# Kernel optimization log

Hardware: AMD Instinct MI355X
Metric: run time of the kernel (lower is better)

## Reference

```python
import jax, jax.numpy as jnp
import numpy as np

NUM_CLASSES = 10
TEMPERATURE = 10.0
EPS = 1e-8


def _centers_counts(feat, label):
    # segment mean per class; counts used for validity masks
    counts = jax.ops.segment_sum(jnp.ones((feat.shape[0],), feat.dtype), label, NUM_CLASSES)
    sums = jax.ops.segment_sum(feat, label, NUM_CLASSES)
    centers = sums / jnp.maximum(counts, 1.0)[:, None]
    return centers, counts


def setup_inputs() -> dict:
    key = jax.random.key(0)
    k1, k2, k3, k4 = jax.random.split(key, 4)
    N, D = 262144, 64
    return {
        "feat1": jax.random.normal(k1, (N, D), dtype=jnp.float32),
        "label1": jax.random.randint(k2, (N,), 0, NUM_CLASSES, dtype=jnp.int32),
        "feat2": jax.random.normal(k3, (N, D), dtype=jnp.float32),
        "label2": jax.random.randint(k4, (N,), 0, NUM_CLASSES, dtype=jnp.int32),
    }


def reference(feat1, label1, feat2, label2):
    centers1, counts1 = _centers_counts(feat1, label1)   # [C, D], [C]
    centers2, counts2 = _centers_counts(feat2, label2)

    # per-sample euclidean distance to own class center
    d1 = jnp.sqrt(jnp.sum((feat1 - centers1[label1]) ** 2, axis=1))  # [N1]
    d2 = jnp.sqrt(jnp.sum((feat2 - centers2[label2]) ** 2, axis=1))  # [N2]

    # per-class mean distances (segment mean)
    m1 = jax.ops.segment_sum(d1, label1, NUM_CLASSES) / jnp.maximum(counts1, 1.0)
    m2 = jax.ops.segment_sum(d2, label2, NUM_CLASSES) / jnp.maximum(counts2, 1.0)

    # intra: only classes (present in label1, as torch.unique(label1)) with >1 members in both
    valid_intra = (counts1 > 1.0) & (counts2 > 1.0)
    intra_dist = jnp.sum(jnp.where(valid_intra, m1 + m2, 0.0))

    # inter: centers for classes present in both domains; mean over all pairwise distances
    valid_c = (counts1 > 0.0) & (counts2 > 0.0)  # [C]
    diff = centers1[:, None, :] - centers2[None, :, :]  # [C, C, D]
    pd = jnp.sqrt(jnp.sum(diff ** 2, axis=-1))           # [C, C]
    w = (valid_c[:, None] & valid_c[None, :]).astype(pd.dtype)
    n_valid = jnp.sum(valid_c.astype(pd.dtype))
    inter_dist = jnp.where(
        n_valid > 1.0,
        jnp.sum(pd * w) / jnp.maximum(n_valid * n_valid, 1.0),
        0.0,
    )

    normalized = intra_dist / (inter_dist + EPS)
    loss = jnp.where(
        inter_dist > 0.0,
        jnp.log1p(jnp.exp(normalized / TEMPERATURE)),
        intra_dist,
    )
    return loss
```

## Files before the change

### kernel.cpp

```cpp
#include <hip/hip_runtime.h>
#include <math.h>

#define NUM_CLASSES 10
#define D 64

#define PART_FLOATS 1320
#define OFF_SUMS1 0
#define OFF_SUMS2 640
#define OFF_CNT1  1280
#define OFF_CNT2  1290
#define OFF_DSUM1 1300
#define OFF_DSUM2 1310
#define CTR_FLOATS 1300
#define CTR_OFF_C1   0
#define CTR_OFF_C2   640
#define CTR_OFF_CNT1 1280
#define CTR_OFF_CNT2 1290

__global__ void k_zero(float* __restrict__ ws, int npart) {
    int total = npart * PART_FLOATS;
    for (int i = threadIdx.x + blockIdx.x * blockDim.x; i < total; i += blockDim.x * gridDim.x)
        ws[i] = 0.0f;
}

__global__ void k_pass1(const float* __restrict__ f1, const int* __restrict__ l1,
                        const float* __restrict__ f2, const int* __restrict__ l2,
                        int N, float* __restrict__ ws, int npart) {
    const float* f; const int* l; int base_s, base_c;
    if (blockIdx.y == 0) { f = f1; l = l1; base_s = OFF_SUMS1; base_c = OFF_CNT1; }
    else                 { f = f2; l = l2; base_s = OFF_SUMS2; base_c = OFF_CNT2; }
    float* wpart = ws + (size_t)(blockIdx.x & (npart - 1)) * PART_FLOATS;

    __shared__ float accum[4][NUM_CLASSES * D];
    __shared__ float cshare[4][16];
    const int wv   = threadIdx.x >> 6;
    const int lane = threadIdx.x & 63;
    float* acc = accum[wv];

    for (int i = threadIdx.x; i < 4 * NUM_CLASSES * D; i += blockDim.x)
        (&accum[0][0])[i] = 0.0f;
    __syncthreads();

    const int wid   = blockIdx.x * 4 + wv;
    const int nwave = gridDim.x * 4;
    float vcnt = 0.0f;

    for (int r0 = wid * 64; r0 < N; r0 += nwave * 64) {
        int labv = l[min(r0 + lane, N - 1)];
        int nrows = min(64, N - r0);
        for (int rr = 0; rr < 64; rr += 16) {
            float v[16];
#pragma unroll
            for (int k = 0; k < 16; ++k) {
                int ra = min(r0 + rr + k, N - 1);
                v[k] = f[(size_t)ra * D + lane];
            }
#pragma unroll
            for (int k = 0; k < 16; ++k) {
                int r = rr + k;
                if (r < nrows) {
                    int lab = __shfl(labv, r);
                    acc[lab * D + lane] += v[k];
                    vcnt += (lane == lab) ? 1.0f : 0.0f;
                }
            }
        }
    }

    if (lane < NUM_CLASSES) cshare[wv][lane] = vcnt;
    __syncthreads();

    for (int i = threadIdx.x; i < NUM_CLASSES * D; i += blockDim.x) {
        float s = accum[0][i] + accum[1][i] + accum[2][i] + accum[3][i];
        atomicAdd(&wpart[base_s + i], s);
    }
    if (threadIdx.x < NUM_CLASSES) {
        float s = cshare[0][threadIdx.x] + cshare[1][threadIdx.x]
                + cshare[2][threadIdx.x] + cshare[3][threadIdx.x];
        atomicAdd(&wpart[base_c + threadIdx.x], s);
    }
}

__global__ void k_centers(const float* __restrict__ ws, int npart, float* __restrict__ gctr) {
    int dom = blockIdx.x;
    int base_s = dom ? OFF_SUMS2 : OFF_SUMS1;
    int base_c = dom ? OFF_CNT2  : OFF_CNT1;
    int out_c  = dom ? CTR_OFF_C2 : CTR_OFF_C1;
    int out_n  = dom ? CTR_OFF_CNT2 : CTR_OFF_CNT1;
    __shared__ float cnts[NUM_CLASSES];
    if (threadIdx.x < NUM_CLASSES) {
        float a0 = 0.f, a1 = 0.f, a2 = 0.f, a3 = 0.f;
        int p = 0;
        for (; p + 4 <= npart; p += 4) {
            a0 += ws[(p + 0) * PART_FLOATS + base_c + threadIdx.x];
            a1 += ws[(p + 1) * PART_FLOATS + base_c + threadIdx.x];
            a2 += ws[(p + 2) * PART_FLOATS + base_c + threadIdx.x];
            a3 += ws[(p + 3) * PART_FLOATS + base_c + threadIdx.x];
        }
        float cn = (a0 + a1) + (a2 + a3);
        for (; p < npart; ++p) cn += ws[p * PART_FLOATS + base_c + threadIdx.x];
        cnts[threadIdx.x] = cn;
        gctr[out_n + threadIdx.x] = cn;
    }
    __syncthreads();
    int i = threadIdx.x;
    if (i < NUM_CLASSES * D) {
        float a0 = 0.f, a1 = 0.f, a2 = 0.f, a3 = 0.f, a4 = 0.f, a5 = 0.f, a6 = 0.f, a7 = 0.f;
        int p = 0;
        for (; p + 8 <= npart; p += 8) {
            a0 += ws[(p + 0) * PART_FLOATS + base_s + i];
            a1 += ws[(p + 1) * PART_FLOATS + base_s + i];
            a2 += ws[(p + 2) * PART_FLOATS + base_s + i];
            a3 += ws[(p + 3) * PART_FLOATS + base_s + i];
            a4 += ws[(p + 4) * PART_FLOATS + base_s + i];
            a5 += ws[(p + 5) * PART_FLOATS + base_s + i];
            a6 += ws[(p + 6) * PART_FLOATS + base_s + i];
            a7 += ws[(p + 7) * PART_FLOATS + base_s + i];
        }
        float s = ((a0 + a1) + (a2 + a3)) + ((a4 + a5) + (a6 + a7));
        for (; p < npart; ++p) s += ws[p * PART_FLOATS + base_s + i];
        gctr[out_c + i] = s / fmaxf(cnts[i >> 6], 1.0f);
    }
}

__global__ void k_pass2(const float* __restrict__ f1, const int* __restrict__ l1,
                        const float* __restrict__ f2, const int* __restrict__ l2,
                        int N, float* __restrict__ ws, int npart,
                        const float* __restrict__ gctr) {
    const float* f; const int* l; int base_d, ctr_off;
    if (blockIdx.y == 0) { f = f1; l = l1; base_d = OFF_DSUM1; ctr_off = CTR_OFF_C1; }
    else                 { f = f2; l = l2; base_d = OFF_DSUM2; ctr_off = CTR_OFF_C2; }
    float* wpart = ws + (size_t)(blockIdx.x & (npart - 1)) * PART_FLOATS;

    __shared__ float4 ctr[NUM_CLASSES * 17];
    __shared__ float  ld[NUM_CLASSES];
    float* ctrf = reinterpret_cast<float*>(ctr);
    for (int i = threadIdx.x; i < NUM_CLASSES * D; i += blockDim.x)
        ctrf[(i >> 6) * 68 + (i & 63)] = gctr[ctr_off + i];
    if (threadIdx.x < NUM_CLASSES) ld[threadIdx.x] = 0.f;
    __syncthreads();

    const int j = threadIdx.x & 3;
    int g       = blockIdx.x * (blockDim.x >> 2) + (threadIdx.x >> 2);
    const int G = gridDim.x * (blockDim.x >> 2);
    const float4* f4 = reinterpret_cast<const float4*>(f);

    for (int row = g; row < N; row += G) {
        int lab = l[row];
        size_t rb = (size_t)row * 16;
        float4 v0 = f4[rb + 0 + j];
        float4 v1 = f4[rb + 4 + j];
        float4 v2 = f4[rb + 8 + j];
        float4 v3 = f4[rb + 12 + j];
        const float4* cc = &ctr[lab * 17];
        float4 c0 = cc[0 + j], c1 = cc[4 + j], c2 = cc[8 + j], c3 = cc[12 + j];
        float s = 0.f, x;
        x = v0.x - c0.x; s = fmaf(x, x, s); x = v0.y - c0.y; s = fmaf(x, x, s);
        x = v0.z - c0.z; s = fmaf(x, x, s); x = v0.w - c0.w; s = fmaf(x, x, s);
        x = v1.x - c1.x; s = fmaf(x, x, s); x = v1.y - c1.y; s = fmaf(x, x, s);
        x = v1.z - c1.z; s = fmaf(x, x, s); x = v1.w - c1.w; s = fmaf(x, x, s);
        x = v2.x - c2.x; s = fmaf(x, x, s); x = v2.y - c2.y; s = fmaf(x, x, s);
        x = v2.z - c2.z; s = fmaf(x, x, s); x = v2.w - c2.w; s = fmaf(x, x, s);
        x = v3.x - c3.x; s = fmaf(x, x, s); x = v3.y - c3.y; s = fmaf(x, x, s);
        x = v3.z - c3.z; s = fmaf(x, x, s); x = v3.w - c3.w; s = fmaf(x, x, s);
        s += __shfl_xor(s, 1);
        s += __shfl_xor(s, 2);
        if (j == 0) atomicAdd(&ld[lab], sqrtf(s));
    }
    __syncthreads();
    if (threadIdx.x < NUM_CLASSES)
        atomicAdd(&wpart[base_d + threadIdx.x], ld[threadIdx.x]);
}

__global__ void k_final(const float* __restrict__ ws, int npart,
                        const float* __restrict__ gctr, float* __restrict__ out) {
    __shared__ float cnt1[NUM_CLASSES], cnt2[NUM_CLASSES], ds1[NUM_CLASSES], ds2[NUM_CLASSES];
    __shared__ float pd[NUM_CLASSES * NUM_CLASSES];

    if (threadIdx.x < 2 * NUM_CLASSES) {
        int which = threadIdx.x / NUM_CLASSES, c = threadIdx.x % NUM_CLASSES;
        int off = (which == 0 ? OFF_DSUM1 : OFF_DSUM2) + c;
        float s = 0.f;
        for (int p = 0; p < npart; ++p) s += ws[p * PART_FLOATS + off];
        (which == 0 ? ds1 : ds2)[c] = s;
        (which == 0 ? cnt1 : cnt2)[c] = gctr[(which == 0 ? CTR_OFF_CNT1 : CTR_OFF_CNT2) + c];
    }
    __syncthreads();

    if (threadIdx.x < NUM_CLASSES * NUM_CLASSES) {
        int i = threadIdx.x / NUM_CLASSES;
        int j = threadIdx.x % NUM_CLASSES;
        float s = 0.f;
        for (int d = 0; d < D; ++d) {
            float df = gctr[CTR_OFF_C1 + i * D + d] - gctr[CTR_OFF_C2 + j * D + d];
            s += df * df;
        }
        pd[threadIdx.x] = sqrtf(s);
    }
    __syncthreads();

    if (threadIdx.x == 0) {
        float intra = 0.f;
        for (int c = 0; c < NUM_CLASSES; ++c) {
            if (cnt1[c] > 1.0f && cnt2[c] > 1.0f) {
                float m1 = ds1[c] / fmaxf(cnt1[c], 1.0f);
                float m2 = ds2[c] / fmaxf(cnt2[c], 1.0f);
                intra += m1 + m2;
            }
        }
        float n_valid = 0.f;
        for (int i = 0; i < NUM_CLASSES; ++i)
            if (cnt1[i] > 0.0f && cnt2[i] > 0.0f) n_valid += 1.0f;
        float inter_sum = 0.f;
        for (int i = 0; i < NUM_CLASSES; ++i) {
            bool vi = cnt1[i] > 0.0f && cnt2[i] > 0.0f;
            for (int j = 0; j < NUM_CLASSES; ++j) {
                bool vj = cnt1[j] > 0.0f && cnt2[j] > 0.0f;
                if (vi && vj) inter_sum += pd[i * NUM_CLASSES + j];
            }
        }
        float inter = (n_valid > 1.0f) ? inter_sum / fmaxf(n_valid * n_valid, 1.0f) : 0.0f;
        float normalized = intra / (inter + 1e-8f);
        float x = normalized / 10.0f;
        float softplus = (x > 0.0f) ? (x + log1pf(expf(-x))) : log1pf(expf(x));
        float loss = (inter > 0.0f) ? softplus : intra;
        out[0] = loss;
    }
}

extern "C" void kernel_launch(void* const* d_in, const int* in_sizes, int n_in,
                              void* d_out, int out_size, void* d_ws, size_t ws_size,
                              hipStream_t stream) {
    const float* f1 = (const float*)d_in[0];
    const int*   l1 = (const int*)d_in[1];
    const float* f2 = (const float*)d_in[2];
    const int*   l2 = (const int*)d_in[3];
    float* ws  = (float*)d_ws;
    float* out = (float*)d_out;
    const int N = in_sizes[1];

    int npart = 1;
    while (npart < 64 &&
           (size_t)(npart * 2 * PART_FLOATS + CTR_FLOATS) * sizeof(float) <= ws_size)
        npart <<= 1;
    float* gctr = ws + (size_t)npart * PART_FLOATS;

    k_zero<<<32, 256, 0, stream>>>(ws, npart);
    dim3 grid1(1024, 2);
    k_pass1<<<grid1, 256, 0, stream>>>(f1, l1, f2, l2, N, ws, npart);
    k_centers<<<2, 640, 0, stream>>>(ws, npart, gctr);
    dim3 grid2(1024, 2);
    k_pass2<<<grid2, 256, 0, stream>>>(f1, l1, f2, l2, N, ws, npart, gctr);
    k_final<<<1, 128, 0, stream>>>(ws, npart, gctr, out);
}
```

Measured before the change: 87.32 us.

## Vectorize pass1 loads to float4 with per-slot padded shared accumulators

Result: no change. 86.57 us (-0.9%).

```diff
diff --git a/kernel.cpp b/kernel.cpp
--- a/kernel.cpp
+++ b/kernel.cpp
@@ -17,6 +17,11 @@
 #define CTR_OFF_CNT1 1280
 #define CTR_OFF_CNT2 1290
 
+#define ACC_CLS_F4   17
+#define ACC_COPY_F4  (NUM_CLASSES * ACC_CLS_F4)
+#define ACC_COPY_F   (ACC_COPY_F4 * 4)
+#define ACC_TOTAL_F4 (16 * ACC_COPY_F4)
+
 __global__ void k_zero(float* __restrict__ ws, int npart) {
     int total = npart * PART_FLOATS;
     for (int i = threadIdx.x + blockIdx.x * blockDim.x; i < total; i += blockDim.x * gridDim.x)
@@ -31,47 +36,79 @@
     else                 { f = f2; l = l2; base_s = OFF_SUMS2; base_c = OFF_CNT2; }
     float* wpart = ws + (size_t)(blockIdx.x & (npart - 1)) * PART_FLOATS;
 
-    __shared__ float accum[4][NUM_CLASSES * D];
-    __shared__ float cshare[4][16];
-    const int wv   = threadIdx.x >> 6;
-    const int lane = threadIdx.x & 63;
-    float* acc = accum[wv];
-
-    for (int i = threadIdx.x; i < 4 * NUM_CLASSES * D; i += blockDim.x)
-        (&accum[0][0])[i] = 0.0f;
+    __shared__ float4 accf4[ACC_TOTAL_F4];
+    __shared__ float  cshare[4][16];
+    const int wv    = threadIdx.x >> 6;
+    const int lane  = threadIdx.x & 63;
+    const int chunk = lane & 15;
+    const int slot  = lane >> 4;
+    float4* acc = accf4 + (wv * 4 + slot) * ACC_COPY_F4;
+
+    for (int i = threadIdx.x; i < ACC_TOTAL_F4; i += blockDim.x)
+        accf4[i] = make_float4(0.f, 0.f, 0.f, 0.f);
     __syncthreads();
 
     const int wid   = blockIdx.x * 4 + wv;
     const int nwave = gridDim.x * 4;
+    const float4* f4p = reinterpret_cast<const float4*>(f);
     float vcnt = 0.0f;
 
     for (int r0 = wid * 64; r0 < N; r0 += nwave * 64) {
         int labv = l[min(r0 + lane, N - 1)];
-        int nrows = min(64, N - r0);
-        for (int rr = 0; rr < 64; rr += 16) {
-            float v[16];
 #pragma unroll
-            for (int k = 0; k < 16; ++k) {
-                int ra = min(r0 + rr + k, N - 1);
-                v[k] = f[(size_t)ra * D + lane];
-            }
+        for (int k4 = 0; k4 < 16; k4 += 4) {
+            int r_0 = r0 + (k4 + 0) * 4 + slot;
+            int r_1 = r0 + (k4 + 1) * 4 + slot;
+            int r_2 = r0 + (k4 + 2) * 4 + slot;
+            int r_3 = r0 + (k4 + 3) * 4 + slot;
+            float w0 = (r_0 < N) ? 1.f : 0.f;  int a_0 = min(r_0, N - 1);
+            float w1 = (r_1 < N) ? 1.f : 0.f;  int a_1 = min(r_1, N - 1);
+            float w2 = (r_2 < N) ? 1.f : 0.f;  int a_2 = min(r_2, N - 1);
+            float w3 = (r_3 < N) ? 1.f : 0.f;  int a_3 = min(r_3, N - 1);
+            float4 v0 = f4p[(size_t)a_0 * 16 + chunk];
+            float4 v1 = f4p[(size_t)a_1 * 16 + chunk];
+            float4 v2 = f4p[(size_t)a_2 * 16 + chunk];
+            float4 v3 = f4p[(size_t)a_3 * 16 + chunk];
+            int lb0 = __shfl(labv, (k4 + 0) * 4 + slot);
+            int lb1 = __shfl(labv, (k4 + 1) * 4 + slot);
+            int lb2 = __shfl(labv, (k4 + 2) * 4 + slot);
+            int lb3 = __shfl(labv, (k4 + 3) * 4 + slot);
+            float4 t;
+            t = acc[lb0 * ACC_CLS_F4 + chunk];
+            t.x = fmaf(w0, v0.x, t.x); t.y = fmaf(w0, v0.y, t.y);
+            t.z = fmaf(w0, v0.z, t.z); t.w = fmaf(w0, v0.w, t.w);
+            acc[lb0 * ACC_CLS_F4 + chunk] = t;
+            vcnt += (chunk == lb0) ? w0 : 0.f;
+            t = acc[lb1 * ACC_CLS_F4 + chunk];
+            t.x = fmaf(w1, v1.x, t.x); t.y = fmaf(w1, v1.y, t.y);
+            t.z = fmaf(w1, v1.z, t.z); t.w = fmaf(w1, v1.w, t.w);
+            acc[lb1 * ACC_CLS_F4 + chunk] = t;
+            vcnt += (chunk == lb1) ? w1 : 0.f;
+            t = acc[lb2 * ACC_CLS_F4 + chunk];
+            t.x = fmaf(w2, v2.x, t.x); t.y = fmaf(w2, v2.y, t.y);
+            t.z = fmaf(w2, v2.z, t.z); t.w = fmaf(w2, v2.w, t.w);
+            acc[lb2 * ACC_CLS_F4 + chunk] = t;
+            vcnt += (chunk == lb2) ? w2 : 0.f;
+            t = acc[lb3 * ACC_CLS_F4 + chunk];
+            t.x = fmaf(w3, v3.x, t.x); t.y = fmaf(w3, v3.y, t.y);
+            t.z = fmaf(w3, v3.z, t.z); t.w = fmaf(w3, v3.w, t.w);
+            acc[lb3 * ACC_CLS_F4 + chunk] = t;
+            vcnt += (chunk == lb3) ? w3 : 0.f;
+        }
+    }
+
+    vcnt += __shfl_xor(vcnt, 16);
+    vcnt += __shfl_xor(vcnt, 32);
+    if (lane < NUM_CLASSES) cshare[wv][lane] = vcnt;
+    __syncthreads();
+
+    const float* accf = reinterpret_cast<const float*>(accf4);
+    for (int i = threadIdx.x; i < NUM_CLASSES * D; i += blockDim.x) {
+        int cls = i >> 6, el = i & 63;
+        float s = 0.f;
 #pragma unroll
-            for (int k = 0; k < 16; ++k) {
-                int r = rr + k;
-                if (r < nrows) {
-                    int lab = __shfl(labv, r);
-                    acc[lab * D + lane] += v[k];
-                    vcnt += (lane == lab) ? 1.0f : 0.0f;
-                }
-            }
-        }
-    }
-
-    if (lane < NUM_CLASSES) cshare[wv][lane] = vcnt;
-    __syncthreads();
-
-    for (int i = threadIdx.x; i < NUM_CLASSES * D; i += blockDim.x) {
-        float s = accum[0][i] + accum[1][i] + accum[2][i] + accum[3][i];
+        for (int cp = 0; cp < 16; ++cp)
+            s += accf[cp * ACC_COPY_F + cls * (ACC_CLS_F4 * 4) + el];
         atomicAdd(&wpart[base_s + i], s);
     }
     if (threadIdx.x < NUM_CLASSES) {
@@ -246,7 +283,7 @@
     float* gctr = ws + (size_t)npart * PART_FLOATS;
 
     k_zero<<<32, 256, 0, stream>>>(ws, npart);
-    dim3 grid1(1024, 2);
+    dim3 grid1(384, 2);
     k_pass1<<<grid1, 256, 0, stream>>>(f1, l1, f2, l2, N, ws, npart);
     k_centers<<<2, 640, 0, stream>>>(ws, npart, gctr);
     dim3 grid2(1024, 2);
```
